# Kernel tuning notes

Measured on AMD Instinct MI355X. Metric: run time of the kernel, lower is better.

## Reference

```python
import jax, jax.numpy as jnp
import numpy as np
from jax import lax

C = 32    # feats_channels
CT = 16   # transform_channels
B, D, H, W = 1, 16, 16, 32  # N = D*H*W = 8192


def _bcast(v):
    return v[None, :, None, None, None]


def conv1(x, w):
    # 1x1x1 Conv3d, no bias: w [O, I], x [b, I, d, h, w]
    return jnp.einsum('oi,bidhw->bodhw', w, x)


def cbr(x, w, s, b):
    # Conv1x1x1 + inference BatchNorm (folded to scale s / bias b) + ReLU
    return jax.nn.relu(conv1(x, w) * _bcast(s) + _bcast(b))


def setup_inputs() -> dict:
    key = jax.random.key(0)
    ks = jax.random.split(key, 16)

    def wmat(k, shape, scale=0.05):
        return jax.random.normal(k, shape, jnp.float32) * scale

    def bn(k, n):
        k1, k2 = jax.random.split(k)
        s = 1.0 + 0.05 * jax.random.normal(k1, (n,), jnp.float32)
        b = 0.05 * jax.random.normal(k2, (n,), jnp.float32)
        return s, b

    inp = {'x': jax.random.normal(ks[0], (B, C, D, H, W), jnp.float32)}
    # query_project: 2 convs (C->CT, CT->CT), each conv+BN+ReLU
    inp['wq1'] = wmat(ks[1], (CT, C));  inp['sq1'], inp['bq1'] = bn(ks[2], CT)
    inp['wq2'] = wmat(ks[3], (CT, CT)); inp['sq2'], inp['bq2'] = bn(ks[4], CT)
    # key_project: 2 convs (2C->CT, CT->CT)
    inp['wk1'] = wmat(ks[5], (CT, 2 * C)); inp['sk1'], inp['bk1'] = bn(ks[6], CT)
    inp['wk2'] = wmat(ks[7], (CT, CT));    inp['sk2'], inp['bk2'] = bn(ks[8], CT)
    # value_project: 1 conv (2C->CT) + BN + ReLU
    inp['wv'] = wmat(ks[9], (CT, 2 * C)); inp['sv'], inp['bv'] = bn(ks[10], CT)
    # out_project: 1 conv (CT->C) + BN + ReLU
    inp['wo'] = wmat(ks[11], (C, CT)); inp['so'], inp['bo'] = bn(ks[12], C)
    # bottleneck: Conv3d(2C->C, k=3, pad=1, no bias) + BN + LeakyReLU(0.1)
    inp['wbot'] = wmat(ks[13], (C, 2 * C, 3, 3, 3), 0.02)
    inp['sbot'], inp['bbot'] = bn(ks[14], C)
    return inp


def reference(x, wq1, sq1, bq1, wq2, sq2, bq2,
              wk1, sk1, bk1, wk2, sk2, bk2,
              wv, sv, bv, wo, so, bo, wbot, sbot, bbot):
    b, c, d, h, w = x.shape
    # AdaptiveAvgPool2d((1,1)) on (b, c*d, h, w) = mean over (h, w) per (c,d);
    # bilinear upsample from 1x1 is a constant broadcast.
    xg = jnp.mean(x, axis=(3, 4), keepdims=True)
    key_feats = jnp.concatenate([jnp.broadcast_to(xg, x.shape), x], axis=1)  # [b, 2c, d, h, w]

    q = cbr(cbr(x, wq1, sq1, bq1), wq2, sq2, bq2)          # [b, CT, d, h, w]
    k = cbr(cbr(key_feats, wk1, sk1, bk1), wk2, sk2, bk2)  # [b, CT, d, h, w]
    v = cbr(key_feats, wv, sv, bv)                          # [b, CT, d, h, w]

    n = d * h * w
    q = q.reshape(b, CT, n).transpose(0, 2, 1)  # [b, N, CT]
    k = k.reshape(b, CT, n)                     # [b, CT, N]
    v = v.reshape(b, CT, n).transpose(0, 2, 1)  # [b, N, CT]

    sim = jnp.einsum('bnc,bcm->bnm', q, k) * (CT ** -0.5)   # [b, N, N]
    sim = jax.nn.softmax(sim, axis=-1)
    ctx = jnp.einsum('bnm,bmc->bnc', sim, v)                # [b, N, CT]
    ctx = ctx.transpose(0, 2, 1).reshape(b, CT, d, h, w)
    ctx = cbr(ctx, wo, so, bo)                              # [b, C, d, h, w]

    fused = jnp.concatenate([x, ctx], axis=1)               # [b, 2C, d, h, w]
    y = lax.conv_general_dilated(
        fused, wbot, window_strides=(1, 1, 1), padding='SAME',
        dimension_numbers=('NCDHW', 'OIDHW', 'NCDHW'))
    y = y * _bcast(sbot) + _bcast(bbot)
    return jnp.where(y > 0, y, 0.1 * y)  # LeakyReLU(0.1)
```

## Files before the change

kernel.cpp:

```cpp
#include <hip/hip_runtime.h>

typedef unsigned int u32;
typedef unsigned short u16;
typedef float f32x16 __attribute__((ext_vector_type(16)));
typedef __bf16 bf16x8 __attribute__((ext_vector_type(8)));
union BF8 { u32 w[4]; bf16x8 v; };

#define DEVI static __device__ __forceinline__
DEVI u32 pk_bf16(float lo, float hi) {
  u32 r;
  asm("v_cvt_pk_bf16_f32 %0, %1, %2" : "=v"(r) : "v"(lo), "v"(hi));
  return r;
}
DEVI u16 bf1(float x) { return (u16)(pk_bf16(x, 0.0f) & 0xffffu); }

#define WB_WREP  0
#define WB_QS    131072
#define WB_K     393216
#define WB_VTS   655360
#define WB_FUS   917504

#define SX_XT   0
#define SX_H0   640
#define SX_H1   912
#define SX_P8   1184
#define SX_XG   1440
#define SX_DKX  1472
#define SX_DVX  1488

__global__ __launch_bounds__(256) void k_prep(
    const float* __restrict__ x,
    const float* __restrict__ wq1, const float* __restrict__ sq1, const float* __restrict__ bq1,
    const float* __restrict__ wq2, const float* __restrict__ sq2, const float* __restrict__ bq2,
    const float* __restrict__ wk1, const float* __restrict__ sk1, const float* __restrict__ bk1,
    const float* __restrict__ wk2, const float* __restrict__ sk2, const float* __restrict__ bk2,
    const float* __restrict__ wv,  const float* __restrict__ sv,  const float* __restrict__ bv,
    const float* __restrict__ wbot, const float* __restrict__ sbot,
    u16* __restrict__ qs, u16* __restrict__ kbm, u16* __restrict__ vts,
    u16* __restrict__ fus, u16* __restrict__ wrep) {
  const int tid = threadIdx.x;
  const int bid = blockIdx.x;
  if (bid >= 512) {
    const int rb = bid - 512;
#pragma unroll
    for (int e = 0; e < 8; ++e) {
      const int idx = rb * 2048 + tid * 8 + e;
      const int tap = idx >> 11, rem = idx & 2047, o = rem >> 6, i = rem & 63;
      wrep[idx] = bf1(wbot[(o * 64 + i) * 27 + tap] * sbot[o]);
    }
    return;
  }
  __shared__ float SH[1504];
  const int n0 = bid << 4;
  const int d = bid >> 5;
  {
    const int c = tid >> 3, part = tid & 7;
    const float4* xp = (const float4*)(x + (c << 13) + (d << 9));
    float s = 0.f;
#pragma unroll
    for (int i = 0; i < 16; ++i) {
      const float4 v4 = xp[part + (i << 3)];
      s += v4.x + v4.y + v4.z + v4.w;
    }
    SH[SX_P8 + (c << 3) + part] = s;
    if (tid < 128) {
      const int cc = tid >> 2, ii = tid & 3;
      const float4 v4 = *(const float4*)(x + (cc << 13) + n0 + (ii << 2));
      *(float4*)(&SH[SX_XT + cc * 20 + (ii << 2)]) = v4;
    }
  }
  __syncthreads();
  if (tid < 32) {
    float s = 0.f;
#pragma unroll
    for (int j = 0; j < 8; ++j) s += SH[SX_P8 + (tid << 3) + j];
    SH[SX_XG + tid] = s * (1.0f / 512.0f);
    const float4* wxf = (tid < 16) ? (const float4*)wk1 : (const float4*)wv;
    const int g = tid & 15;
    float dx = 0.f;
#pragma unroll
    for (int c4 = 0; c4 < 8; ++c4) {
      const float4 wa = wxf[g * 16 + c4];
      dx += wa.x * SH[SX_XG + 4*c4] + wa.y * SH[SX_XG + 4*c4+1] +
            wa.z * SH[SX_XG + 4*c4+2] + wa.w * SH[SX_XG + 4*c4+3];
    }
    SH[(tid < 16 ? SX_DKX : SX_DVX - 16) + tid] = dx;
  }
  __syncthreads();
  const int nl = tid & 15, g = tid >> 4;
  const int n = n0 + nl;
  {
    float xc[32];
#pragma unroll
    for (int c = 0; c < 32; ++c) xc[c] = SH[SX_XT + c * 20 + nl];
    const float4* wq1f = (const float4*)wq1;
    const float4* wk1f = (const float4*)wk1;
    const float4* wvf  = (const float4*)wv;
    float dq = 0.f, dk = SH[SX_DKX + g], dv = SH[SX_DVX + g];
#pragma unroll
    for (int c4 = 0; c4 < 8; ++c4) {
      const float4 wa = wq1f[g * 8 + c4];
      dq += wa.x * xc[4*c4+0] + wa.y * xc[4*c4+1] + wa.z * xc[4*c4+2] + wa.w * xc[4*c4+3];
      const float4 ka = wk1f[g * 16 + 8 + c4];
      dk += ka.x * xc[4*c4+0] + ka.y * xc[4*c4+1] + ka.z * xc[4*c4+2] + ka.w * xc[4*c4+3];
      const float4 va = wvf[g * 16 + 8 + c4];
      dv += va.x * xc[4*c4+0] + va.y * xc[4*c4+1] + va.z * xc[4*c4+2] + va.w * xc[4*c4+3];
    }
    const float hq = fmaxf(dq * sq1[g] + bq1[g], 0.f);
    const float hk = fmaxf(dk * sk1[g] + bk1[g], 0.f);
    const float hv = fmaxf(dv * sv[g] + bv[g], 0.f);
    SH[SX_H0 + nl * 17 + g] = hq;
    SH[SX_H1 + nl * 17 + g] = hk;
    vts[((n >> 5) << 9) + (g << 5) + (n & 31)] = bf1(hv);
    const int c0 = g << 1;
    *(u32*)(fus + (n << 6) + c0) = pk_bf16(SH[SX_XT + c0 * 20 + nl],
                                           SH[SX_XT + (c0 + 1) * 20 + nl]);
  }
  __syncthreads();
  {
    const int op = tid >> 4;
    const bool isq = (op < 8);
    const int r0 = (op & 7) << 1, r1 = r0 + 1;
    const float* w2 = isq ? wq2 : wk2;
    const float* Hrow = &SH[(isq ? SX_H0 : SX_H1) + nl * 17];
    float e0 = 0.f, e1 = 0.f;
#pragma unroll
    for (int j = 0; j < 16; ++j) {
      const float hv2 = Hrow[j];
      e0 += w2[r0 * 16 + j] * hv2;
      e1 += w2[r1 * 16 + j] * hv2;
    }
    if (isq) {
      const float SC = 0.36067376022224085f;
      const float q0 = fmaxf(e0 * (sq2[r0] * SC) + bq2[r0] * SC, 0.f);
      const float q1 = fmaxf(e1 * (sq2[r1] * SC) + bq2[r1] * SC, 0.f);
      *(u32*)(qs + (n << 4) + r0) = pk_bf16(q0, q1);
    } else {
      const float k0 = fmaxf(e0 * sk2[r0] + bk2[r0], 0.f);
      const float k1 = fmaxf(e1 * sk2[r1] + bk2[r1], 0.f);
      *(u32*)(kbm + (n << 4) + r0) = pk_bf16(k0, k1);
    }
  }
}

__global__ __launch_bounds__(1024) void k_attn(
    const u16* __restrict__ qs, const u16* __restrict__ kbm, const u16* __restrict__ vts,
    const float* __restrict__ wo, const float* __restrict__ so, const float* __restrict__ bo,
    u16* __restrict__ fus) {
  __shared__ float R[16][32][17];
  const int tid = threadIdx.x;
  const int w = tid >> 6, lane = tid & 63;
  const int l31 = lane & 31, h = lane >> 5;
  const int qb = blockIdx.x;

  const bf16x8 qf = *(const bf16x8*)(qs + (((qb << 5) + l31) << 4) + (h << 3));
  f32x16 acc_a, acc_b, z;
#pragma unroll
  for (int i = 0; i < 16; ++i) { acc_a[i] = 0.f; acc_b[i] = 0.f; z[i] = 0.f; }

  const u32 fill = (l31 == 16) ? 0x3F803F80u : 0u;
  const int kb0 = w << 9;
  const int t0 = w << 4;
  const bool vlane = (l31 < 16);
  const u16* vbase = vts + (l31 << 5) + (h << 3);
  const u16* krow = kbm + (l31 << 4) + (h << 3);

  bf16x8 kf_c = *(const bf16x8*)(krow + (kb0 << 4));
  BF8 V1c, V2c;
#pragma unroll
  for (int j2 = 0; j2 < 4; ++j2) { V1c.w[j2] = fill; V2c.w[j2] = fill; }
  if (vlane) {
    V1c.v = *(const bf16x8*)(vbase + (t0 << 9));
    V2c.v = *(const bf16x8*)(vbase + (t0 << 9) + 16);
  }
  f32x16 st = __builtin_amdgcn_mfma_f32_32x32x16_bf16(kf_c, qf, z, 0, 0, 0);
  kf_c = *(const bf16x8*)(krow + ((kb0 + 32) << 4));

#pragma unroll
  for (int t = 0; t < 16; ++t) {
    f32x16 st_next;
    if (t < 15) st_next = __builtin_amdgcn_mfma_f32_32x32x16_bf16(kf_c, qf, z, 0, 0, 0);
    const BF8 V1 = V1c, V2 = V2c;
    if (t < 14) kf_c = *(const bf16x8*)(krow + ((kb0 + ((t + 2) << 5)) << 4));
    if (t < 15 && vlane) {
      const u16* vp = vbase + ((t0 + t + 1) << 9);
      V1c.v = *(const bf16x8*)vp;
      V2c.v = *(const bf16x8*)(vp + 16);
    }
    float pe[16];
#pragma unroll
    for (int r = 0; r < 8; ++r) pe[r] = __builtin_amdgcn_exp2f(st[r]);
    u32 a0 = pk_bf16(pe[0], pe[1]), a1 = pk_bf16(pe[2], pe[3]);
    u32 a2 = pk_bf16(pe[4], pe[5]), a3 = pk_bf16(pe[6], pe[7]);
    asm("v_permlane32_swap_b32 %0, %1" : "+v"(a0), "+v"(a2));
    asm("v_permlane32_swap_b32 %0, %1" : "+v"(a1), "+v"(a3));
    BF8 A1;
    A1.w[0] = a0; A1.w[1] = a1; A1.w[2] = a2; A1.w[3] = a3;
    __builtin_amdgcn_s_setprio(1);
    acc_a = __builtin_amdgcn_mfma_f32_32x32x16_bf16(A1.v, V1.v, acc_a, 0, 0, 0);
    __builtin_amdgcn_s_setprio(0);
#pragma unroll
    for (int r = 8; r < 16; ++r) pe[r] = __builtin_amdgcn_exp2f(st[r]);
    u32 b0 = pk_bf16(pe[8],  pe[9]),  b1 = pk_bf16(pe[10], pe[11]);
    u32 b2 = pk_bf16(pe[12], pe[13]), b3 = pk_bf16(pe[14], pe[15]);
    asm("v_permlane32_swap_b32 %0, %1" : "+v"(b0), "+v"(b2));
    asm("v_permlane32_swap_b32 %0, %1" : "+v"(b1), "+v"(b3));
    BF8 A2;
    A2.w[0] = b0; A2.w[1] = b1; A2.w[2] = b2; A2.w[3] = b3;
    __builtin_amdgcn_s_setprio(1);
    acc_b = __builtin_amdgcn_mfma_f32_32x32x16_bf16(A2.v, V2.v, acc_b, 0, 0, 0);
    __builtin_amdgcn_s_setprio(0);
    if (t < 15) st = st_next;
  }
  if (l31 < 17) {
#pragma unroll
    for (int r = 0; r < 16; ++r) {
      const int row = (r & 3) + ((r >> 2) << 3) + (h << 2);
      R[w][row][l31] = acc_a[r] + acc_b[r];
    }
  }
  __syncthreads();
  float* Rf = &R[0][0][0];
  if (tid < 544) {
    float s0 = 0.f;
#pragma unroll
    for (int w2 = 0; w2 < 16; ++w2) s0 += Rf[w2 * 544 + tid];
    Rf[tid] = s0;
  }
  __syncthreads();
  if (tid < 512) {
    const int row = tid >> 4;
    const int o0 = (tid & 15) << 1, o1 = o0 + 1;
    const float inv = 1.0f / Rf[row * 17 + 16];
    float d0 = 0.f, d1 = 0.f;
#pragma unroll
    for (int c = 0; c < 16; ++c) {
      const float cv = Rf[row * 17 + c];
      d0 += wo[o0 * 16 + c] * cv;
      d1 += wo[o1 * 16 + c] * cv;
    }
    const float y0 = fmaxf(bo[o0] + so[o0] * d0 * inv, 0.f);
    const float y1 = fmaxf(bo[o1] + so[o1] * d1 * inv, 0.f);
    *(u32*)(fus + (((qb << 5) + row) << 6) + 32 + o0) = pk_bf16(y0, y1);
  }
}

__global__ __launch_bounds__(512) void k_conv(
    const u16* __restrict__ fus, const u16* __restrict__ wrep,
    const float* __restrict__ bbot, float* __restrict__ out) {
  __shared__ float R8[8][1024];
  const int tid = threadIdx.x;
  const int wv = tid >> 6, lane = tid & 63;
  const int l31 = lane & 31, h = lane >> 5;
  const int n0 = blockIdx.x << 5;
  const int dz = n0 >> 9, hy = (n0 >> 5) & 15;
  f32x16 acc0, acc1;
#pragma unroll
  for (int i = 0; i < 16; ++i) { acc0[i] = 0.f; acc1[i] = 0.f; }
  const int ulo = (wv * 54) >> 3, uhi = ((wv + 1) * 54) >> 3;

  const u16* bp_c; const u16* wp_c; bool ok_c;
  {
    const int tap = ulo >> 1, ch = (ulo & 1) << 1;
    const int dd = tap / 9 - 1, dh = (tap / 3) % 3 - 1, dw = tap % 3 - 1;
    ok_c = ((unsigned)(dz + dd) < 16u) & ((unsigned)(hy + dh) < 16u) &
           ((unsigned)(l31 + dw) < 32u);
    const int nn = n0 + dd * 512 + dh * 32 + dw + l31;
    bp_c = fus + (nn << 6) + (ch << 4) + (h << 3);
    wp_c = wrep + ((tap * 32 + l31) << 6) + (ch << 4) + (h << 3);
  }
  BF8 B0c, B1c;
  B0c.w[0] = B0c.w[1] = B0c.w[2] = B0c.w[3] = 0u;
  B1c.w[0] = B1c.w[1] = B1c.w[2] = B1c.w[3] = 0u;
  if (ok_c) { B0c.v = *(const bf16x8*)bp_c; B1c.v = *(const bf16x8*)(bp_c + 16); }

  for (int u = ulo; u < uhi; ++u) {
    const BF8 B0 = B0c, B1 = B1c;
    const u16* wp = wp_c;
    if (u + 1 < uhi) {
      const int un = u + 1;
      const int tap = un >> 1, ch = (un & 1) << 1;
      const int dd = tap / 9 - 1, dh = (tap / 3) % 3 - 1, dw = tap % 3 - 1;
      const bool ok = ((unsigned)(dz + dd) < 16u) & ((unsigned)(hy + dh) < 16u) &
                      ((unsigned)(l31 + dw) < 32u);
      const int nn = n0 + dd * 512 + dh * 32 + dw + l31;
      const u16* bp = fus + (nn << 6) + (ch << 4) + (h << 3);
      wp_c = wrep + ((tap * 32 + l31) << 6) + (ch << 4) + (h << 3);
      B0c.w[0] = B0c.w[1] = B0c.w[2] = B0c.w[3] = 0u;
      B1c.w[0] = B1c.w[1] = B1c.w[2] = B1c.w[3] = 0u;
      if (ok) { B0c.v = *(const bf16x8*)bp; B1c.v = *(const bf16x8*)(bp + 16); }
    }
    const bf16x8 af0 = *(const bf16x8*)wp;
    const bf16x8 af1 = *(const bf16x8*)(wp + 16);
    __builtin_amdgcn_s_setprio(1);
    acc0 = __builtin_amdgcn_mfma_f32_32x32x16_bf16(af0, B0.v, acc0, 0, 0, 0);
    acc1 = __builtin_amdgcn_mfma_f32_32x32x16_bf16(af1, B1.v, acc1, 0, 0, 0);
    __builtin_amdgcn_s_setprio(0);
  }
#pragma unroll
  for (int r = 0; r < 16; ++r) {
    const int row = (r & 3) + ((r >> 2) << 3) + (h << 2);
    R8[wv][(row << 5) + l31] = acc0[r] + acc1[r];
  }
  __syncthreads();
#pragma unroll
  for (int k2 = 0; k2 < 2; ++k2) {
    const int e = tid + (k2 << 9);
    const int row = e >> 5;
    float yv = bbot[row];
#pragma unroll
    for (int w2 = 0; w2 < 8; ++w2) yv += R8[w2][e];
    out[(row << 13) + n0 + (e & 31)] = yv > 0.f ? yv : 0.1f * yv;
  }
}

extern "C" void kernel_launch(void* const* d_in, const int* in_sizes, int n_in,
                              void* d_out, int out_size, void* d_ws, size_t ws_size,
                              hipStream_t stream) {
  const float* x    = (const float*)d_in[0];
  const float* wq1  = (const float*)d_in[1];
  const float* sq1  = (const float*)d_in[2];
  const float* bq1  = (const float*)d_in[3];
  const float* wq2  = (const float*)d_in[4];
  const float* sq2  = (const float*)d_in[5];
  const float* bq2  = (const float*)d_in[6];
  const float* wk1  = (const float*)d_in[7];
  const float* sk1  = (const float*)d_in[8];
  const float* bk1  = (const float*)d_in[9];
  const float* wk2  = (const float*)d_in[10];
  const float* sk2  = (const float*)d_in[11];
  const float* bk2  = (const float*)d_in[12];
  const float* wv   = (const float*)d_in[13];
  const float* sv   = (const float*)d_in[14];
  const float* bv   = (const float*)d_in[15];
  const float* wo   = (const float*)d_in[16];
  const float* so   = (const float*)d_in[17];
  const float* bo   = (const float*)d_in[18];
  const float* wbot = (const float*)d_in[19];
  const float* sbot = (const float*)d_in[20];
  const float* bbot = (const float*)d_in[21];
  (void)in_sizes; (void)n_in; (void)out_size; (void)ws_size;

  char* wsb = (char*)d_ws;
  u16* wrep = (u16*)(wsb + WB_WREP);
  u16* qs   = (u16*)(wsb + WB_QS);
  u16* kbm  = (u16*)(wsb + WB_K);
  u16* vts  = (u16*)(wsb + WB_VTS);
  u16* fus  = (u16*)(wsb + WB_FUS);
  float* out = (float*)d_out;

  k_prep<<<539, 256, 0, stream>>>(x, wq1, sq1, bq1, wq2, sq2, bq2,
                                  wk1, sk1, bk1, wk2, sk2, bk2,
                                  wv, sv, bv, wbot, sbot,
                                  qs, kbm, vts, fus, wrep);
  k_attn<<<256, 1024, 0, stream>>>(qs, kbm, vts, wo, so, bo, fus);
  k_conv<<<256, 512, 0, stream>>>(fus, wrep, bbot, out);
}
```

Measured before the change: 33.45 us.

## Double-buffer attention key tiles into two independent ping-pong softmax streams

The attention inner loop now processes two 32-key tiles per iteration, each with its own score MFMA, exp2/pack chain and PV accumulator, and prefetches the next pair of K and V fragments one iteration ahead. The next score MFMA is issued between the exp/permlane work and the PV MFMAs so matrix and vector work can overlap across two independent chains. It also adds a min-waves-per-EU launch bound hint and drops the setprio hints in both attention and the bottleneck conv loop. The extra in-flight fragments and accumulators raise register pressure, and the launch bound hint may force spills.

```diff
diff --git a/kernel.cpp b/kernel.cpp
--- a/kernel.cpp
+++ b/kernel.cpp
@@ -143,7 +143,7 @@
   }
 }
 
-__global__ __launch_bounds__(1024) void k_attn(
+__global__ __launch_bounds__(1024, 4) void k_attn(
     const u16* __restrict__ qs, const u16* __restrict__ kbm, const u16* __restrict__ vts,
     const float* __restrict__ wo, const float* __restrict__ so, const float* __restrict__ bo,
     u16* __restrict__ fus) {
@@ -165,52 +165,85 @@
   const u16* vbase = vts + (l31 << 5) + (h << 3);
   const u16* krow = kbm + (l31 << 4) + (h << 3);
 
-  bf16x8 kf_c = *(const bf16x8*)(krow + (kb0 << 4));
-  BF8 V1c, V2c;
-#pragma unroll
-  for (int j2 = 0; j2 < 4; ++j2) { V1c.w[j2] = fill; V2c.w[j2] = fill; }
+  bf16x8 kfA = *(const bf16x8*)(krow + (kb0 << 4));
+  bf16x8 kfB = *(const bf16x8*)(krow + ((kb0 + 32) << 4));
+  BF8 VA1, VA2, VB1, VB2;
+#pragma unroll
+  for (int j2 = 0; j2 < 4; ++j2) {
+    VA1.w[j2] = fill; VA2.w[j2] = fill; VB1.w[j2] = fill; VB2.w[j2] = fill;
+  }
   if (vlane) {
-    V1c.v = *(const bf16x8*)(vbase + (t0 << 9));
-    V2c.v = *(const bf16x8*)(vbase + (t0 << 9) + 16);
-  }
-  f32x16 st = __builtin_amdgcn_mfma_f32_32x32x16_bf16(kf_c, qf, z, 0, 0, 0);
-  kf_c = *(const bf16x8*)(krow + ((kb0 + 32) << 4));
-
-#pragma unroll
-  for (int t = 0; t < 16; ++t) {
-    f32x16 st_next;
-    if (t < 15) st_next = __builtin_amdgcn_mfma_f32_32x32x16_bf16(kf_c, qf, z, 0, 0, 0);
-    const BF8 V1 = V1c, V2 = V2c;
-    if (t < 14) kf_c = *(const bf16x8*)(krow + ((kb0 + ((t + 2) << 5)) << 4));
-    if (t < 15 && vlane) {
-      const u16* vp = vbase + ((t0 + t + 1) << 9);
-      V1c.v = *(const bf16x8*)vp;
-      V2c.v = *(const bf16x8*)(vp + 16);
-    }
-    float pe[16];
-#pragma unroll
-    for (int r = 0; r < 8; ++r) pe[r] = __builtin_amdgcn_exp2f(st[r]);
-    u32 a0 = pk_bf16(pe[0], pe[1]), a1 = pk_bf16(pe[2], pe[3]);
-    u32 a2 = pk_bf16(pe[4], pe[5]), a3 = pk_bf16(pe[6], pe[7]);
-    asm("v_permlane32_swap_b32 %0, %1" : "+v"(a0), "+v"(a2));
-    asm("v_permlane32_swap_b32 %0, %1" : "+v"(a1), "+v"(a3));
-    BF8 A1;
-    A1.w[0] = a0; A1.w[1] = a1; A1.w[2] = a2; A1.w[3] = a3;
-    __builtin_amdgcn_s_setprio(1);
-    acc_a = __builtin_amdgcn_mfma_f32_32x32x16_bf16(A1.v, V1.v, acc_a, 0, 0, 0);
-    __builtin_amdgcn_s_setprio(0);
-#pragma unroll
-    for (int r = 8; r < 16; ++r) pe[r] = __builtin_amdgcn_exp2f(st[r]);
-    u32 b0 = pk_bf16(pe[8],  pe[9]),  b1 = pk_bf16(pe[10], pe[11]);
-    u32 b2 = pk_bf16(pe[12], pe[13]), b3 = pk_bf16(pe[14], pe[15]);
-    asm("v_permlane32_swap_b32 %0, %1" : "+v"(b0), "+v"(b2));
-    asm("v_permlane32_swap_b32 %0, %1" : "+v"(b1), "+v"(b3));
-    BF8 A2;
-    A2.w[0] = b0; A2.w[1] = b1; A2.w[2] = b2; A2.w[3] = b3;
-    __builtin_amdgcn_s_setprio(1);
-    acc_b = __builtin_amdgcn_mfma_f32_32x32x16_bf16(A2.v, V2.v, acc_b, 0, 0, 0);
-    __builtin_amdgcn_s_setprio(0);
-    if (t < 15) st = st_next;
+    VA1.v = *(const bf16x8*)(vbase + (t0 << 9));
+    VA2.v = *(const bf16x8*)(vbase + (t0 << 9) + 16);
+    VB1.v = *(const bf16x8*)(vbase + ((t0 + 1) << 9));
+    VB2.v = *(const bf16x8*)(vbase + ((t0 + 1) << 9) + 16);
+  }
+  f32x16 st0 = __builtin_amdgcn_mfma_f32_32x32x16_bf16(kfA, qf, z, 0, 0, 0);
+  f32x16 st1 = __builtin_amdgcn_mfma_f32_32x32x16_bf16(kfB, qf, z, 0, 0, 0);
+
+#pragma unroll
+  for (int j = 0; j < 8; ++j) {
+    bf16x8 kfAn, kfBn;
+    BF8 VA1n, VA2n, VB1n, VB2n;
+    if (j < 7) {
+      const int kbn = kb0 + ((j + 1) << 6);
+      kfAn = *(const bf16x8*)(krow + (kbn << 4));
+      kfBn = *(const bf16x8*)(krow + ((kbn + 32) << 4));
+#pragma unroll
+      for (int j2 = 0; j2 < 4; ++j2) {
+        VA1n.w[j2] = fill; VA2n.w[j2] = fill; VB1n.w[j2] = fill; VB2n.w[j2] = fill;
+      }
+      if (vlane) {
+        const u16* vpA = vbase + ((t0 + 2 * j + 2) << 9);
+        VA1n.v = *(const bf16x8*)vpA;
+        VA2n.v = *(const bf16x8*)(vpA + 16);
+        const u16* vpB = vbase + ((t0 + 2 * j + 3) << 9);
+        VB1n.v = *(const bf16x8*)vpB;
+        VB2n.v = *(const bf16x8*)(vpB + 16);
+      }
+    }
+    {
+      float pe[16];
+#pragma unroll
+      for (int r = 0; r < 16; ++r) pe[r] = __builtin_amdgcn_exp2f(st0[r]);
+      u32 a0 = pk_bf16(pe[0],  pe[1]),  a1 = pk_bf16(pe[2],  pe[3]);
+      u32 a2 = pk_bf16(pe[4],  pe[5]),  a3 = pk_bf16(pe[6],  pe[7]);
+      u32 b0 = pk_bf16(pe[8],  pe[9]),  b1 = pk_bf16(pe[10], pe[11]);
+      u32 b2 = pk_bf16(pe[12], pe[13]), b3 = pk_bf16(pe[14], pe[15]);
+      asm("v_permlane32_swap_b32 %0, %1" : "+v"(a0), "+v"(a2));
+      asm("v_permlane32_swap_b32 %0, %1" : "+v"(a1), "+v"(a3));
+      asm("v_permlane32_swap_b32 %0, %1" : "+v"(b0), "+v"(b2));
+      asm("v_permlane32_swap_b32 %0, %1" : "+v"(b1), "+v"(b3));
+      if (j < 7) st0 = __builtin_amdgcn_mfma_f32_32x32x16_bf16(kfAn, qf, z, 0, 0, 0);
+      BF8 A1, A2;
+      A1.w[0] = a0; A1.w[1] = a1; A1.w[2] = a2; A1.w[3] = a3;
+      A2.w[0] = b0; A2.w[1] = b1; A2.w[2] = b2; A2.w[3] = b3;
+      acc_a = __builtin_amdgcn_mfma_f32_32x32x16_bf16(A1.v, VA1.v, acc_a, 0, 0, 0);
+      acc_a = __builtin_amdgcn_mfma_f32_32x32x16_bf16(A2.v, VA2.v, acc_a, 0, 0, 0);
+    }
+    {
+      float pe[16];
+#pragma unroll
+      for (int r = 0; r < 16; ++r) pe[r] = __builtin_amdgcn_exp2f(st1[r]);
+      u32 a0 = pk_bf16(pe[0],  pe[1]),  a1 = pk_bf16(pe[2],  pe[3]);
+      u32 a2 = pk_bf16(pe[4],  pe[5]),  a3 = pk_bf16(pe[6],  pe[7]);
+      u32 b0 = pk_bf16(pe[8],  pe[9]),  b1 = pk_bf16(pe[10], pe[11]);
+      u32 b2 = pk_bf16(pe[12], pe[13]), b3 = pk_bf16(pe[14], pe[15]);
+      asm("v_permlane32_swap_b32 %0, %1" : "+v"(a0), "+v"(a2));
+      asm("v_permlane32_swap_b32 %0, %1" : "+v"(a1), "+v"(a3));
+      asm("v_permlane32_swap_b32 %0, %1" : "+v"(b0), "+v"(b2));
+      asm("v_permlane32_swap_b32 %0, %1" : "+v"(b1), "+v"(b3));
+      if (j < 7) st1 = __builtin_amdgcn_mfma_f32_32x32x16_bf16(kfBn, qf, z, 0, 0, 0);
+      BF8 B1, B2;
+      B1.w[0] = a0; B1.w[1] = a1; B1.w[2] = a2; B1.w[3] = a3;
+      B2.w[0] = b0; B2.w[1] = b1; B2.w[2] = b2; B2.w[3] = b3;
+      acc_b = __builtin_amdgcn_mfma_f32_32x32x16_bf16(B1.v, VB1.v, acc_b, 0, 0, 0);
+      acc_b = __builtin_amdgcn_mfma_f32_32x32x16_bf16(B2.v, VB2.v, acc_b, 0, 0, 0);
+    }
+    if (j < 7) {
+      kfA = kfAn; kfB = kfBn;
+      VA1 = VA1n; VA2 = VA2n; VB1 = VB1n; VB2 = VB2n;
+    }
   }
   if (l31 < 17) {
 #pragma unroll
@@ -292,10 +325,8 @@
     }
     const bf16x8 af0 = *(const bf16x8*)wp;
     const bf16x8 af1 = *(const bf16x8*)(wp + 16);
-    __builtin_amdgcn_s_setprio(1);
     acc0 = __builtin_amdgcn_mfma_f32_32x32x16_bf16(af0, B0.v, acc0, 0, 0, 0);
     acc1 = __builtin_amdgcn_mfma_f32_32x32x16_bf16(af1, B1.v, acc1, 0, 0, 0);
-    __builtin_amdgcn_s_setprio(0);
   }
 #pragma unroll
   for (int r = 0; r < 16; ++r) {
```

Measured after the change: 34.74 us. +3.9%, slower.
